# Kernel optimization log

Hardware: AMD Instinct MI355X
Metric: run time of the kernel (lower is better)

## Reference

```python
import jax, jax.numpy as jnp
import numpy as np

EPS = 1e-5  # BatchNorm3d default eps


def conv1x1(x, w, b):
    # x: (b, cin, t, h, w); w: (cout, cin); b: (cout,)
    return jnp.einsum('bcthw,oc->bothw', x, w) + b[None, :, None, None, None]


def batchnorm(x):
    # BatchNorm3d(affine=False), training mode: per-channel batch stats over (B,T,H,W)
    mean = jnp.mean(x, axis=(0, 2, 3, 4), keepdims=True)
    var = jnp.var(x, axis=(0, 2, 3, 4), keepdims=True)
    return (x - mean) * jax.lax.rsqrt(var + EPS)


def setup_inputs() -> dict:
    key = jax.random.key(0)
    ks = jax.random.split(key, 9)
    B, C, T, H, W = 4, 512, 16, 14, 14
    IC = C // 4
    s_in = 1.0 / np.sqrt(C)
    s_up = 1.0 / np.sqrt(IC)
    return {
        'maps':    jax.random.normal(ks[0], (B, C, T, H, W), jnp.float32),
        'w_theta': jax.random.uniform(ks[1], (IC, C), jnp.float32, -s_in, s_in),
        'b_theta': jax.random.uniform(ks[2], (IC,),   jnp.float32, -s_in, s_in),
        'w_phalt': jax.random.uniform(ks[3], (IC, C), jnp.float32, -s_in, s_in),
        'b_phalt': jax.random.uniform(ks[4], (IC,),   jnp.float32, -s_in, s_in),
        'w_glob':  jax.random.uniform(ks[5], (IC, C), jnp.float32, -s_in, s_in),
        'b_glob':  jax.random.uniform(ks[6], (IC,),   jnp.float32, -s_in, s_in),
        'w_up':    jax.random.uniform(ks[7], (C, IC), jnp.float32, -s_up, s_up),
        'b_up':    jax.random.uniform(ks[8], (C,),    jnp.float32, -s_up, s_up),
    }


def reference(maps, w_theta, b_theta, w_phalt, b_phalt, w_glob, b_glob, w_up, b_up):
    b, c, t, h, w = maps.shape
    ic = c // 4
    n = t * h * w

    theta_maps = batchnorm(conv1x1(maps, w_theta, b_theta))   # (b, ic, t, h, w)
    phalt_maps = batchnorm(conv1x1(maps, w_phalt, b_phalt))   # computed but UNUSED (bug in original)
    global_maps = batchnorm(conv1x1(maps, w_glob, b_glob))

    theta_x = theta_maps.reshape(b, ic, n)                    # (b, ic, n)
    # NOTE: original code uses theta_maps for phalt_x (faithful to source bug)
    relation = jnp.einsum('bcn,bcm->bnm', theta_x, theta_x)   # (b, n, n)
    relation_normalize = jax.nn.softmax(relation / n, axis=-1)

    global_x = global_maps.reshape(b, ic, n)                  # (b, ic, n)
    y = jnp.einsum('bnm,bcm->bcn', relation_normalize, global_x)
    y = y.reshape(b, ic, t, h, w)

    out = conv1x1(y, w_up, b_up) + maps
    return out
```

## Files before the change

kernel.cpp:

```cpp
#include <hip/hip_runtime.h>
#include <hip/hip_bf16.h>


typedef __attribute__((ext_vector_type(8))) short bf16x8;
typedef __attribute__((ext_vector_type(4))) float f32x4;
typedef __attribute__((ext_vector_type(4))) short s16x4;
typedef __attribute__((ext_vector_type(2))) unsigned int u32x2;

#define NTOK 3136
#define NELEM 1605632
#define NSPLIT 4

__device__ inline float bf2f(short u) {
    union { unsigned int i; float f; } v;
    v.i = ((unsigned int)(unsigned short)u) << 16;
    return v.f;
}
__device__ inline short f2bf(float x) {
    union { float f; unsigned int i; } v;
    v.f = x;
    unsigned int r = v.i + 0x7FFFu + ((v.i >> 16) & 1u);
    return (short)(r >> 16);
}
__device__ inline unsigned int tbf(float x) {
    union { float f; unsigned int i; } v;
    v.f = x;
    return v.i >> 16;
}
__device__ inline void glds16(const void* g, void* l) {
    __builtin_amdgcn_global_load_lds((const __attribute__((address_space(1))) void*)g,
                                     (__attribute__((address_space(3))) void*)l, 16, 0, 0);
}

__global__ __launch_bounds__(256) void prep_w(const float* __restrict__ wt,
                                              const float* __restrict__ wg,
                                              const float* __restrict__ wup,
                                              short* __restrict__ Wb,
                                              short* __restrict__ wupb)
{
    const int i = blockIdx.x * 256 + threadIdx.x;
    if (i < 131072) {
        const int r = i >> 9;
        const int c = i & 511;
        const float w = (r < 128) ? wt[(size_t)r * 512 + c] : wg[(size_t)(r - 128) * 512 + c];
        Wb[i] = f2bf(w);
    } else {
        const int j = i - 131072;
        wupb[j] = f2bf(wup[j]);
    }
}

__global__ __launch_bounds__(256) void conv_in_f(const float* __restrict__ maps,
                                                 const short* __restrict__ Wb,
                                                 short* __restrict__ Tt,
                                                 short* __restrict__ Gpre,
                                                 float* __restrict__ psum,
                                                 float* __restrict__ psq)
{
    const int nt = blockIdx.x, b = blockIdx.y;
    const int n0 = nt * 32;
    const int t = threadIdx.x;
    const int w = __builtin_amdgcn_readfirstlane(t >> 6);
    const int lane = t & 63;
    const int l15 = lane & 15, lhi = lane >> 4;

    __shared__ short Bt[32][136];

    const float* mp = maps + (size_t)b * 512 * NTOK + n0;
    const int cl = t >> 3;
    const int f4 = t & 7;

    f32x4 acc[4][2];
#pragma unroll
    for (int g = 0; g < 4; g++)
#pragma unroll
        for (int j = 0; j < 2; j++) acc[g][j] = f32x4{0.f, 0.f, 0.f, 0.f};

    f32x4 rg[4];
#pragma unroll
    for (int p = 0; p < 4; p++)
        rg[p] = *(const f32x4*)(mp + (size_t)(p * 32 + cl) * NTOK + f4 * 4);

    for (int kc = 0; kc < 4; kc++) {
        __syncthreads();
#pragma unroll
        for (int p = 0; p < 4; p++) {
            const int cc = p * 32 + cl;
#pragma unroll
            for (int i = 0; i < 4; i++) Bt[f4 * 4 + i][cc] = f2bf(rg[p][i]);
        }
        if (kc < 3) {
#pragma unroll
            for (int p = 0; p < 4; p++)
                rg[p] = *(const f32x4*)(mp + (size_t)((kc + 1) * 128 + p * 32 + cl) * NTOK + f4 * 4);
        }
        __syncthreads();
#pragma unroll
        for (int ks = 0; ks < 4; ks++) {
            bf16x8 af[4], bv[2];
#pragma unroll
            for (int g = 0; g < 4; g++)
                af[g] = *(const bf16x8*)(Wb + (size_t)(w * 64 + g * 16 + l15) * 512 + kc * 128 + ks * 32 + lhi * 8);
#pragma unroll
            for (int j = 0; j < 2; j++)
                bv[j] = *(const bf16x8*)(&Bt[j * 16 + l15][ks * 32 + lhi * 8]);
#pragma unroll
            for (int g = 0; g < 4; g++)
#pragma unroll
                for (int j = 0; j < 2; j++)
                    acc[g][j] = __builtin_amdgcn_mfma_f32_16x16x32_bf16(af[g], bv[j], acc[g][j], 0, 0, 0);
        }
    }

    if (w < 2) {
#pragma unroll
        for (int g = 0; g < 4; g++)
#pragma unroll
            for (int j = 0; j < 2; j++) {
                s16x4 v;
#pragma unroll
                for (int r = 0; r < 4; r++) v[r] = f2bf(acc[g][j][r]);
                *(s16x4*)(Tt + ((size_t)b * NTOK + n0 + j * 16 + l15) * 128 + w * 64 + g * 16 + lhi * 4) = v;
            }
    } else {
#pragma unroll
        for (int g = 0; g < 4; g++)
#pragma unroll
            for (int j = 0; j < 2; j++)
#pragma unroll
                for (int r = 0; r < 4; r++) {
                    const int icg = (w - 2) * 64 + g * 16 + lhi * 4 + r;
                    Gpre[((size_t)b * 128 + icg) * NTOK + n0 + j * 16 + l15] = f2bf(acc[g][j][r]);
                }
    }
#pragma unroll
    for (int g = 0; g < 4; g++)
#pragma unroll
        for (int r = 0; r < 4; r++) {
            float s = acc[g][0][r] + acc[g][1][r];
            float q = acc[g][0][r] * acc[g][0][r] + acc[g][1][r] * acc[g][1][r];
#pragma unroll
            for (int off = 1; off < 16; off <<= 1) {
                s += __shfl_xor(s, off);
                q += __shfl_xor(q, off);
            }
            if (l15 == 0) {
                const int ch = w * 64 + g * 16 + lhi * 4 + r;
                psum[(size_t)ch * 392 + b * 98 + nt] = s;
                psq [(size_t)ch * 392 + b * 98 + nt] = q;
            }
        }
}

__global__ __launch_bounds__(64) void stats_fin(const float* __restrict__ psum,
                                                const float* __restrict__ psq,
                                                float* __restrict__ st)
{
    const int ch = blockIdx.x;
    const int lane = threadIdx.x;
    float s = 0.f, q = 0.f;
    for (int i = lane; i < 392; i += 64) {
        s += psum[(size_t)ch * 392 + i];
        q += psq [(size_t)ch * 392 + i];
    }
#pragma unroll
    for (int off = 32; off; off >>= 1) { s += __shfl_xor(s, off); q += __shfl_xor(q, off); }
    if (lane == 0) {
        const float mean = s / 12544.f;
        const float var = q / 12544.f - mean * mean;
        st[ch] = mean;
        st[256 + ch] = rsqrtf(var + 1e-5f);
    }
}

__global__ __launch_bounds__(256) void norm_tg(const short* __restrict__ Tt,
                                               const short* __restrict__ Gpre,
                                               const float* __restrict__ st,
                                               short* __restrict__ Tb,
                                               short* __restrict__ Gb)
{
    const size_t base = ((size_t)blockIdx.x * 256 + threadIdx.x) * 8;
    if (blockIdx.y == 0) {
        const int ic = (int)(base & 127);
        const f32x4 m0 = *(const f32x4*)(st + ic);
        const f32x4 m1 = *(const f32x4*)(st + ic + 4);
        const f32x4 r0 = *(const f32x4*)(st + 256 + ic);
        const f32x4 r1 = *(const f32x4*)(st + 256 + ic + 4);
        bf16x8 v = *(const bf16x8*)(Tt + base);
        bf16x8 o;
#pragma unroll
        for (int j = 0; j < 4; j++) o[j] = f2bf((bf2f(v[j]) - m0[j]) * r0[j]);
#pragma unroll
        for (int j = 0; j < 4; j++) o[4 + j] = f2bf((bf2f(v[4 + j]) - m1[j]) * r1[j]);
        *(bf16x8*)(Tb + base) = o;
    } else {
        const int ic = (int)((base / NTOK) & 127);
        const float mean = st[128 + ic], rstd = st[384 + ic];
        bf16x8 v = *(const bf16x8*)(Gpre + base);
        bf16x8 o;
#pragma unroll
        for (int j = 0; j < 8; j++) o[j] = f2bf((bf2f(v[j]) - mean) * rstd);
        *(bf16x8*)(Gb + base) = o;
    }
}

__global__ __launch_bounds__(256) void attn_k(const short* __restrict__ Tb,
                                              const short* __restrict__ Gb,
                                              float* __restrict__ Opart,
                                              float* __restrict__ dpart)
{
    constexpr int N = NTOK;
    const int b = blockIdx.y, s = blockIdx.z;
    const int w = __builtin_amdgcn_readfirstlane(threadIdx.x >> 6);
    const int lane = threadIdx.x & 63;
    const int l15 = lane & 15, lhi = lane >> 4;
    const int q0w = blockIdx.x * 128 + w * 32;

    __shared__ __align__(16) short Kl[2][64][128];
    __shared__ __align__(16) short Vl[2][128][64];
    __shared__ __align__(16) short Pl[4][32][64];

    const short* tb = Tb + (size_t)b * N * 128;
    const short* gb = Gb + (size_t)b * 128 * N;

    bf16x8 qf[2][4];
#pragma unroll
    for (int qs = 0; qs < 2; qs++) {
        int row = q0w + qs * 16 + l15;
        row = row < N ? row : N - 1;
#pragma unroll
        for (int ks = 0; ks < 4; ks++)
            qf[qs][ks] = *(const bf16x8*)(tb + (size_t)row * 128 + ks * 32 + lhi * 8);
    }

    f32x4 acc[2][8];
#pragma unroll
    for (int qs = 0; qs < 2; qs++)
#pragma unroll
        for (int is = 0; is < 8; is++) acc[qs][is] = f32x4{0.f, 0.f, 0.f, 0.f};
    float denom[2] = {0.f, 0.f};
    const float inv_n = 1.0f / (float)N;

    auto STAGE = [&](int bufi, int m0) {
#pragma unroll
        for (int i = 0; i < 4; i++) {
            const int rb = w * 16 + i * 4;
            const int krow = rb + (lane >> 4);
            const int ksw = ((lane & 15) * 16) ^ ((krow & 7) << 4);
            glds16((const char*)tb + (size_t)(m0 + krow) * 256 + ksw, (char*)&Kl[bufi][rb][0]);
        }
#pragma unroll
        for (int i = 0; i < 4; i++) {
            const int rb = w * 32 + i * 8;
            const int vrow = rb + (lane >> 3);
            const int vsw = ((lane & 7) * 16) ^ ((vrow & 7) << 4);
            glds16((const char*)gb + ((size_t)vrow * N + m0) * 2 + vsw, (char*)&Vl[bufi][rb][0]);
        }
    };

    const int nt = (49 - s + NSPLIT - 1) / NSPLIT;
    int mt = s;
    STAGE(0, mt * 64);
    __syncthreads();
    int buf = 0;

    const int fK = (l15 & 7) << 4;

    for (int t = 0; t < nt; ++t) {
        if (t + 1 < nt) STAGE(buf ^ 1, (mt + NSPLIT) * 64);

        f32x4 sv[2][4];
#pragma unroll
        for (int qs = 0; qs < 2; qs++)
#pragma unroll
            for (int ms = 0; ms < 4; ms++) sv[qs][ms] = f32x4{0.f, 0.f, 0.f, 0.f};
#pragma unroll
        for (int ms = 0; ms < 4; ms++) {
            const char* kbase = (const char*)&Kl[buf][ms * 16 + l15][0];
#pragma unroll
            for (int ks = 0; ks < 4; ks++) {
                bf16x8 kf = *(const bf16x8*)(kbase + ((ks * 64 + lhi * 16) ^ fK));
                sv[0][ms] = __builtin_amdgcn_mfma_f32_16x16x32_bf16(kf, qf[0][ks], sv[0][ms], 0, 0, 0);
                sv[1][ms] = __builtin_amdgcn_mfma_f32_16x16x32_bf16(kf, qf[1][ks], sv[1][ms], 0, 0, 0);
            }
        }
#pragma unroll
        for (int qs = 0; qs < 2; qs++) {
            char* pbase = (char*)&Pl[w][qs * 16 + l15][0];
#pragma unroll
            for (int ms = 0; ms < 4; ms++) {
                const float p0 = __expf(sv[qs][ms][0] * inv_n);
                const float p1 = __expf(sv[qs][ms][1] * inv_n);
                const float p2 = __expf(sv[qs][ms][2] * inv_n);
                const float p3 = __expf(sv[qs][ms][3] * inv_n);
                denom[qs] += (p0 + p1) + (p2 + p3);
                u32x2 u;
                u[0] = tbf(p0) | (tbf(p1) << 16);
                u[1] = tbf(p2) | (tbf(p3) << 16);
                *(u32x2*)(pbase + ((ms * 32 + lhi * 8) ^ fK)) = u;
            }
        }
#pragma unroll
        for (int kp = 0; kp < 2; kp++) {
            const int coff = kp * 64 + lhi * 16;
            bf16x8 pa[2];
#pragma unroll
            for (int qs = 0; qs < 2; qs++)
                pa[qs] = *(const bf16x8*)((const char*)&Pl[w][qs * 16 + l15][0] + (coff ^ fK));
#pragma unroll
            for (int is = 0; is < 8; is++) {
                bf16x8 vf = *(const bf16x8*)((const char*)&Vl[buf][is * 16 + l15][0] + (coff ^ fK));
                acc[0][is] = __builtin_amdgcn_mfma_f32_16x16x32_bf16(pa[0], vf, acc[0][is], 0, 0, 0);
                acc[1][is] = __builtin_amdgcn_mfma_f32_16x16x32_bf16(pa[1], vf, acc[1][is], 0, 0, 0);
            }
        }
        __syncthreads();
        buf ^= 1;
        mt += NSPLIT;
    }

#pragma unroll
    for (int qs = 0; qs < 2; qs++) {
        denom[qs] += __shfl_xor(denom[qs], 16);
        denom[qs] += __shfl_xor(denom[qs], 32);
    }

    float* op = Opart + ((size_t)(s * 4 + b)) * N * 128;
#pragma unroll
    for (int qs = 0; qs < 2; qs++)
#pragma unroll
        for (int is = 0; is < 8; is++)
#pragma unroll
            for (int r = 0; r < 4; r++) {
                const int n = q0w + qs * 16 + lhi * 4 + r;
                if (n < N) op[(size_t)n * 128 + is * 16 + l15] = acc[qs][is][r];
            }
    if (lhi == 0) {
#pragma unroll
        for (int qs = 0; qs < 2; qs++) {
            const int n = q0w + qs * 16 + l15;
            if (n < N) dpart[(size_t)(s * 4 + b) * N + n] = denom[qs];
        }
    }
}

__global__ __launch_bounds__(256) void combine_k(const float* __restrict__ Opart,
                                                 const float* __restrict__ dpart,
                                                 short* __restrict__ Yt)
{
    const int t = blockIdx.x * 256 + threadIdx.x;
    const int ic = (t & 15) * 8;
    const int rest = t >> 4;
    const int n = rest % NTOK;
    const int b = rest / NTOK;
    float sum[8] = {0.f, 0.f, 0.f, 0.f, 0.f, 0.f, 0.f, 0.f};
    float den = 0.f;
#pragma unroll
    for (int s = 0; s < NSPLIT; s++) {
        const size_t base = ((size_t)(s * 4 + b) * NTOK + n) * 128 + ic;
        const f32x4 a = *(const f32x4*)(Opart + base);
        const f32x4 c = *(const f32x4*)(Opart + base + 4);
#pragma unroll
        for (int j = 0; j < 4; j++) { sum[j] += a[j]; sum[4 + j] += c[j]; }
        den += dpart[(size_t)(s * 4 + b) * NTOK + n];
    }
    const float rd = 1.0f / den;
    bf16x8 o;
#pragma unroll
    for (int j = 0; j < 8; j++) o[j] = f2bf(sum[j] * rd);
    *(bf16x8*)(Yt + ((size_t)b * NTOK + n) * 128 + ic) = o;
}

__global__ __launch_bounds__(256) void conv_out_m(const short* __restrict__ Yt,
                                                  const short* __restrict__ wupb,
                                                  const float* __restrict__ bup,
                                                  const float* __restrict__ maps,
                                                  float* __restrict__ out)
{
    const int n0 = blockIdx.x * 32, b = blockIdx.y;
    const int wv = __builtin_amdgcn_readfirstlane(threadIdx.x >> 6);
    const int lane = threadIdx.x & 63;
    const int l15 = lane & 15, lhi = lane >> 4;
    const int c0 = wv * 128;
    const short* yp = Yt + (size_t)b * NTOK * 128;

    f32x4 acc[8][2];
#pragma unroll
    for (int g = 0; g < 8; g++)
#pragma unroll
        for (int j = 0; j < 2; j++) acc[g][j] = f32x4{0.f, 0.f, 0.f, 0.f};

#pragma unroll
    for (int ks = 0; ks < 4; ks++) {
        const int k0 = ks * 32 + lhi * 8;
        bf16x8 af[8], bf[2];
#pragma unroll
        for (int g = 0; g < 8; g++)
            af[g] = *(const bf16x8*)(wupb + (size_t)(c0 + g * 16 + l15) * 128 + k0);
#pragma unroll
        for (int j = 0; j < 2; j++)
            bf[j] = *(const bf16x8*)(yp + (size_t)(n0 + j * 16 + l15) * 128 + k0);
#pragma unroll
        for (int g = 0; g < 8; g++)
#pragma unroll
            for (int j = 0; j < 2; j++)
                acc[g][j] = __builtin_amdgcn_mfma_f32_16x16x32_bf16(af[g], bf[j], acc[g][j], 0, 0, 0);
    }
#pragma unroll
    for (int g = 0; g < 8; g++)
#pragma unroll
        for (int j = 0; j < 2; j++)
#pragma unroll
            for (int r = 0; r < 4; r++) {
                const int c = c0 + g * 16 + lhi * 4 + r;
                const int n = n0 + j * 16 + l15;
                const size_t o = ((size_t)b * 512 + c) * NTOK + n;
                out[o] = acc[g][j][r] + bup[c] + maps[o];
            }
}

extern "C" void kernel_launch(void* const* d_in, const int* in_sizes, int n_in,
                              void* d_out, int out_size, void* d_ws, size_t ws_size,
                              hipStream_t stream)
{
    const float* maps    = (const float*)d_in[0];
    const float* w_theta = (const float*)d_in[1];
    const float* w_glob  = (const float*)d_in[5];
    const float* w_up    = (const float*)d_in[7];
    const float* b_up    = (const float*)d_in[8];
    float* out = (float*)d_out;

    short* Tt    = (short*)d_ws;
    short* Gpre  = Tt + NELEM;
    short* Tb    = Gpre + NELEM;
    short* Gb    = Tb + NELEM;
    short* Yt    = Gb + NELEM;
    short* Wb    = Yt + NELEM;
    short* wupb  = Wb + 131072;
    float* st    = (float*)(wupb + 65536);
    float* psum  = st + 512;
    float* psq   = psum + 100352;
    float* dpart = psq + 100352;
    float* Opart = out;

    prep_w    <<<768,             256, 0, stream>>>(w_theta, w_glob, w_up, Wb, wupb);
    conv_in_f <<<dim3(98, 4),     256, 0, stream>>>(maps, Wb, Tt, Gpre, psum, psq);
    stats_fin <<<256,             64,  0, stream>>>(psum, psq, st);
    norm_tg   <<<dim3(784, 2),    256, 0, stream>>>(Tt, Gpre, st, Tb, Gb);
    attn_k    <<<dim3(25, 4, NSPLIT), 256, 0, stream>>>(Tb, Gb, Opart, dpart);
    combine_k <<<784,             256, 0, stream>>>(Opart, dpart, Yt);
    conv_out_m<<<dim3(98, 4),     256, 0, stream>>>(Yt, wupb, b_up, maps, out);
}
```

Baseline: 98.07 us.

## Fold BatchNorm into attention via softmax shift-invariance and fuse combine into output conv

```diff
diff --git a/kernel.cpp b/kernel.cpp
--- a/kernel.cpp
+++ b/kernel.cpp
@@ -173,39 +173,9 @@
     }
 }
 
-__global__ __launch_bounds__(256) void norm_tg(const short* __restrict__ Tt,
-                                               const short* __restrict__ Gpre,
-                                               const float* __restrict__ st,
-                                               short* __restrict__ Tb,
-                                               short* __restrict__ Gb)
-{
-    const size_t base = ((size_t)blockIdx.x * 256 + threadIdx.x) * 8;
-    if (blockIdx.y == 0) {
-        const int ic = (int)(base & 127);
-        const f32x4 m0 = *(const f32x4*)(st + ic);
-        const f32x4 m1 = *(const f32x4*)(st + ic + 4);
-        const f32x4 r0 = *(const f32x4*)(st + 256 + ic);
-        const f32x4 r1 = *(const f32x4*)(st + 256 + ic + 4);
-        bf16x8 v = *(const bf16x8*)(Tt + base);
-        bf16x8 o;
-#pragma unroll
-        for (int j = 0; j < 4; j++) o[j] = f2bf((bf2f(v[j]) - m0[j]) * r0[j]);
-#pragma unroll
-        for (int j = 0; j < 4; j++) o[4 + j] = f2bf((bf2f(v[4 + j]) - m1[j]) * r1[j]);
-        *(bf16x8*)(Tb + base) = o;
-    } else {
-        const int ic = (int)((base / NTOK) & 127);
-        const float mean = st[128 + ic], rstd = st[384 + ic];
-        bf16x8 v = *(const bf16x8*)(Gpre + base);
-        bf16x8 o;
-#pragma unroll
-        for (int j = 0; j < 8; j++) o[j] = f2bf((bf2f(v[j]) - mean) * rstd);
-        *(bf16x8*)(Gb + base) = o;
-    }
-}
-
-__global__ __launch_bounds__(256) void attn_k(const short* __restrict__ Tb,
-                                              const short* __restrict__ Gb,
+__global__ __launch_bounds__(256) void attn_k(const short* __restrict__ Tt,
+                                              const short* __restrict__ Gpre,
+                                              const float* __restrict__ st,
                                               float* __restrict__ Opart,
                                               float* __restrict__ dpart)
 {
@@ -220,8 +190,8 @@
     __shared__ __align__(16) short Vl[2][128][64];
     __shared__ __align__(16) short Pl[4][32][64];
 
-    const short* tb = Tb + (size_t)b * N * 128;
-    const short* gb = Gb + (size_t)b * 128 * N;
+    const short* tb = Tt + (size_t)b * N * 128;
+    const short* gb = Gpre + (size_t)b * 128 * N;
 
     bf16x8 qf[2][4];
 #pragma unroll
@@ -229,8 +199,20 @@
         int row = q0w + qs * 16 + l15;
         row = row < N ? row : N - 1;
 #pragma unroll
-        for (int ks = 0; ks < 4; ks++)
-            qf[qs][ks] = *(const bf16x8*)(tb + (size_t)row * 128 + ks * 32 + lhi * 8);
+        for (int ks = 0; ks < 4; ks++) {
+            const bf16x8 v = *(const bf16x8*)(tb + (size_t)row * 128 + ks * 32 + lhi * 8);
+            const int c0 = ks * 32 + lhi * 8;
+            const f32x4 mA = *(const f32x4*)(st + c0);
+            const f32x4 mB = *(const f32x4*)(st + c0 + 4);
+            const f32x4 rA = *(const f32x4*)(st + 256 + c0);
+            const f32x4 rB = *(const f32x4*)(st + 256 + c0 + 4);
+            bf16x8 q;
+#pragma unroll
+            for (int j = 0; j < 4; j++) q[j] = f2bf((bf2f(v[j]) - mA[j]) * (rA[j] * rA[j]));
+#pragma unroll
+            for (int j = 0; j < 4; j++) q[4 + j] = f2bf((bf2f(v[4 + j]) - mB[j]) * (rB[j] * rB[j]));
+            qf[qs][ks] = q;
+        }
     }
 
     f32x4 acc[2][8];
@@ -344,45 +326,63 @@
     }
 }
 
-__global__ __launch_bounds__(256) void combine_k(const float* __restrict__ Opart,
-                                                 const float* __restrict__ dpart,
-                                                 short* __restrict__ Yt)
-{
-    const int t = blockIdx.x * 256 + threadIdx.x;
-    const int ic = (t & 15) * 8;
-    const int rest = t >> 4;
-    const int n = rest % NTOK;
-    const int b = rest / NTOK;
-    float sum[8] = {0.f, 0.f, 0.f, 0.f, 0.f, 0.f, 0.f, 0.f};
-    float den = 0.f;
-#pragma unroll
-    for (int s = 0; s < NSPLIT; s++) {
-        const size_t base = ((size_t)(s * 4 + b) * NTOK + n) * 128 + ic;
-        const f32x4 a = *(const f32x4*)(Opart + base);
-        const f32x4 c = *(const f32x4*)(Opart + base + 4);
-#pragma unroll
-        for (int j = 0; j < 4; j++) { sum[j] += a[j]; sum[4 + j] += c[j]; }
-        den += dpart[(size_t)(s * 4 + b) * NTOK + n];
-    }
-    const float rd = 1.0f / den;
-    bf16x8 o;
-#pragma unroll
-    for (int j = 0; j < 8; j++) o[j] = f2bf(sum[j] * rd);
-    *(bf16x8*)(Yt + ((size_t)b * NTOK + n) * 128 + ic) = o;
-}
-
-__global__ __launch_bounds__(256) void conv_out_m(const short* __restrict__ Yt,
+__global__ __launch_bounds__(256) void conv_out_f(const float* __restrict__ Opart,
+                                                  const float* __restrict__ dpart,
+                                                  const float* __restrict__ st,
                                                   const short* __restrict__ wupb,
                                                   const float* __restrict__ bup,
                                                   const float* __restrict__ maps,
                                                   float* __restrict__ out)
 {
     const int n0 = blockIdx.x * 32, b = blockIdx.y;
-    const int wv = __builtin_amdgcn_readfirstlane(threadIdx.x >> 6);
-    const int lane = threadIdx.x & 63;
+    const int t = threadIdx.x;
+
+    __shared__ float denl[32];
+    __shared__ __align__(16) short Yl[32][128];
+
+    if (t < 32) {
+        float d = 0.f;
+#pragma unroll
+        for (int s = 0; s < NSPLIT; s++) d += dpart[(size_t)(s * 4 + b) * NTOK + n0 + t];
+        denl[t] = 1.0f / d;
+    }
+    __syncthreads();
+
+#pragma unroll
+    for (int g = 0; g < 2; g++) {
+        const int e = t + g * 256;
+        const int nl = e >> 4, icg = (e & 15) * 8;
+        const float rdn = denl[nl];
+        float sum[8] = {0.f, 0.f, 0.f, 0.f, 0.f, 0.f, 0.f, 0.f};
+#pragma unroll
+        for (int s = 0; s < NSPLIT; s++) {
+            const size_t base = ((size_t)(s * 4 + b) * NTOK + n0 + nl) * 128 + icg;
+            const f32x4 a = *(const f32x4*)(Opart + base);
+            const f32x4 c = *(const f32x4*)(Opart + base + 4);
+#pragma unroll
+            for (int j = 0; j < 4; j++) { sum[j] += a[j]; sum[4 + j] += c[j]; }
+        }
+        const f32x4 mA = *(const f32x4*)(st + 128 + icg);
+        const f32x4 mB = *(const f32x4*)(st + 128 + icg + 4);
+        const f32x4 rA = *(const f32x4*)(st + 384 + icg);
+        const f32x4 rB = *(const f32x4*)(st + 384 + icg + 4);
+        s16x4 v0, v1;
+#pragma unroll
+        for (int j = 0; j < 4; j++) v0[j] = f2bf((sum[j] * rdn - mA[j]) * rA[j]);
+#pragma unroll
+        for (int j = 0; j < 4; j++) v1[j] = f2bf((sum[4 + j] * rdn - mB[j]) * rB[j]);
+        char* ybase = (char*)&Yl[nl][0];
+        const int sw = (nl & 7) << 4;
+        *(s16x4*)(ybase + ((icg * 2) ^ sw)) = v0;
+        *(s16x4*)(ybase + (((icg * 2) ^ sw) + 8)) = v1;
+    }
+    __syncthreads();
+
+    const int wv = __builtin_amdgcn_readfirstlane(t >> 6);
+    const int lane = t & 63;
     const int l15 = lane & 15, lhi = lane >> 4;
     const int c0 = wv * 128;
-    const short* yp = Yt + (size_t)b * NTOK * 128;
+    const int fY = (l15 & 7) << 4;
 
     f32x4 acc[8][2];
 #pragma unroll
@@ -392,19 +392,18 @@
 
 #pragma unroll
     for (int ks = 0; ks < 4; ks++) {
-        const int k0 = ks * 32 + lhi * 8;
-        bf16x8 af[8], bf[2];
+        bf16x8 af[8], bv[2];
 #pragma unroll
         for (int g = 0; g < 8; g++)
-            af[g] = *(const bf16x8*)(wupb + (size_t)(c0 + g * 16 + l15) * 128 + k0);
+            af[g] = *(const bf16x8*)(wupb + (size_t)(c0 + g * 16 + l15) * 128 + ks * 32 + lhi * 8);
 #pragma unroll
         for (int j = 0; j < 2; j++)
-            bf[j] = *(const bf16x8*)(yp + (size_t)(n0 + j * 16 + l15) * 128 + k0);
+            bv[j] = *(const bf16x8*)((const char*)&Yl[j * 16 + l15][0] + ((ks * 64 + lhi * 16) ^ fY));
 #pragma unroll
         for (int g = 0; g < 8; g++)
 #pragma unroll
             for (int j = 0; j < 2; j++)
-                acc[g][j] = __builtin_amdgcn_mfma_f32_16x16x32_bf16(af[g], bf[j], acc[g][j], 0, 0, 0);
+                acc[g][j] = __builtin_amdgcn_mfma_f32_16x16x32_bf16(af[g], bv[j], acc[g][j], 0, 0, 0);
     }
 #pragma unroll
     for (int g = 0; g < 8; g++)
@@ -432,22 +431,17 @@
 
     short* Tt    = (short*)d_ws;
     short* Gpre  = Tt + NELEM;
-    short* Tb    = Gpre + NELEM;
-    short* Gb    = Tb + NELEM;
-    short* Yt    = Gb + NELEM;
-    short* Wb    = Yt + NELEM;
+    short* Wb    = Gpre + NELEM;
     short* wupb  = Wb + 131072;
     float* st    = (float*)(wupb + 65536);
     float* psum  = st + 512;
     float* psq   = psum + 100352;
     float* dpart = psq + 100352;
-    float* Opart = out;
+    float* Opart = dpart + 50176;
 
     prep_w    <<<768,             256, 0, stream>>>(w_theta, w_glob, w_up, Wb, wupb);
     conv_in_f <<<dim3(98, 4),     256, 0, stream>>>(maps, Wb, Tt, Gpre, psum, psq);
     stats_fin <<<256,             64,  0, stream>>>(psum, psq, st);
-    norm_tg   <<<dim3(784, 2),    256, 0, stream>>>(Tt, Gpre, st, Tb, Gb);
-    attn_k    <<<dim3(25, 4, NSPLIT), 256, 0, stream>>>(Tb, Gb, Opart, dpart);
-    combine_k <<<784,             256, 0, stream>>>(Opart, dpart, Yt);
-    conv_out_m<<<dim3(98, 4),     256, 0, stream>>>(Yt, wupb, b_up, maps, out);
-}
+    attn_k    <<<dim3(25, 4, NSPLIT), 256, 0, stream>>>(Tt, Gpre, st, Opart, dpart);
+    conv_out_f<<<dim3(98, 4),     256, 0, stream>>>(Opart, dpart, st, wupb, b_up, maps, out);
+}
```

New measurement: 91.88 us. 1.07x faster.
